# Kernel optimization log

Hardware: AMD Instinct MI355X
Metric: run time of the kernel (lower is better)

The kernel has to match this reference:

```python
import jax, jax.numpy as jnp
import numpy as np

N_NODES = 100000
N_EDGES = 3200000
D_IN = 16
D_OUT = 32


def setup_inputs() -> dict:
    key = jax.random.key(0)
    ks = jax.random.split(key, 8)
    x = jax.random.normal(ks[0], (N_NODES, D_IN), dtype=jnp.float32)
    edge_index = jax.random.randint(ks[1], (2, N_EDGES), 0, N_NODES, dtype=jnp.int64)
    s = 1.0 / np.sqrt(D_IN)
    # mlp1: Linear(16,16) -> ReLU -> Linear(16,16)
    w1 = jax.random.uniform(ks[2], (D_IN, D_IN), jnp.float32, -s, s)
    b1 = jax.random.uniform(ks[3], (D_IN,), jnp.float32, -s, s)
    w2 = jax.random.uniform(ks[4], (D_IN, D_IN), jnp.float32, -s, s)
    b2 = jax.random.uniform(ks[5], (D_IN,), jnp.float32, -s, s)
    # SAGEConv(16,32): lin_l (neighbors, with bias), lin_r (root, no bias)
    wl = jax.random.uniform(ks[6], (D_IN, D_OUT), jnp.float32, -s, s)
    bl = jnp.zeros((D_OUT,), jnp.float32)
    wr = jax.random.uniform(ks[7], (D_IN, D_OUT), jnp.float32, -s, s)
    return {"x": x, "edge_index": edge_index, "w1": w1, "b1": b1,
            "w2": w2, "b2": b2, "wl": wl, "bl": bl, "wr": wr}


def reference(x, edge_index, w1, b1, w2, b2, wl, bl, wr):
    # MLP: Linear -> ReLU -> Linear
    h = jax.nn.relu(x @ w1 + b1) @ w2 + b2  # [N, 16]
    src, dst = edge_index[0], edge_index[1]
    # mean aggregation of neighbor (source) features at destination nodes
    msg = h[src]  # [E, 16]
    summed = jax.ops.segment_sum(msg, dst, num_segments=N_NODES)  # [N, 16]
    cnt = jax.ops.segment_sum(jnp.ones((msg.shape[0],), h.dtype), dst,
                              num_segments=N_NODES)
    mean = summed / jnp.maximum(cnt, 1.0)[:, None]
    # SAGEConv: lin_l(aggr) + lin_r(root)
    out = mean @ wl + bl + h @ wr  # [N, 32]
    return out
```

## Files before the change

### kernel.cpp

```cpp
#include <hip/hip_runtime.h>
#include <hip/hip_bf16.h>

#define D_IN_C 16
#define BUCKET_SHIFT 9
#define BUCKET_NODES 512
#define CAP 18432
#define PT 16
#define PART_CHUNK 4096

__global__ __launch_bounds__(256) void mlp_kernel(
    const float* __restrict__ x,
    const float* __restrict__ w1, const float* __restrict__ b1,
    const float* __restrict__ w2, const float* __restrict__ b2,
    float* __restrict__ h, int* __restrict__ bcur,
    int n_nodes) {
  __shared__ float sw1[256];
  __shared__ float sw2[256];
  __shared__ float sb1[16];
  __shared__ float sb2[16];
  int t = threadIdx.x;
  if (blockIdx.x == 0) bcur[t] = 0;
  sw1[t] = w1[t];
  sw2[t] = w2[t];
  if (t < 16) { sb1[t] = b1[t]; sb2[t] = b2[t]; }
  __syncthreads();

  int n = blockIdx.x * blockDim.x + t;
  if (n >= n_nodes) return;

  float xi[16];
  const float4* xr = (const float4*)(x + (size_t)n * 16);
  float4 v0 = xr[0], v1 = xr[1], v2 = xr[2], v3 = xr[3];
  xi[0]=v0.x; xi[1]=v0.y; xi[2]=v0.z; xi[3]=v0.w;
  xi[4]=v1.x; xi[5]=v1.y; xi[6]=v1.z; xi[7]=v1.w;
  xi[8]=v2.x; xi[9]=v2.y; xi[10]=v2.z; xi[11]=v2.w;
  xi[12]=v3.x; xi[13]=v3.y; xi[14]=v3.z; xi[15]=v3.w;

  float t1[16];
#pragma unroll
  for (int j = 0; j < 16; ++j) {
    float acc = sb1[j];
#pragma unroll
    for (int k = 0; k < 16; ++k) acc += xi[k] * sw1[k * 16 + j];
    t1[j] = fmaxf(acc, 0.0f);
  }
  float hh[16];
#pragma unroll
  for (int j = 0; j < 16; ++j) {
    float acc = sb2[j];
#pragma unroll
    for (int k = 0; k < 16; ++k) acc += t1[k] * sw2[k * 16 + j];
    hh[j] = acc;
  }

  float4* hw = (float4*)(h + (size_t)n * 16);
  hw[0] = make_float4(hh[0], hh[1], hh[2], hh[3]);
  hw[1] = make_float4(hh[4], hh[5], hh[6], hh[7]);
  hw[2] = make_float4(hh[8], hh[9], hh[10], hh[11]);
  hw[3] = make_float4(hh[12], hh[13], hh[14], hh[15]);
}

__global__ __launch_bounds__(256) void part_kernel(
    const int* __restrict__ src, const int* __restrict__ dst,
    int* __restrict__ bcur, int* __restrict__ part,
    int* __restrict__ cnt, int nbuck, int n_edges) {
  __shared__ int lhist[256];
  __shared__ int lofs[256];
  int t = threadIdx.x;
  int base = blockIdx.x * PART_CHUNK;

  int zi = blockIdx.x * 256 + t;
  if (zi < nbuck * BUCKET_NODES) cnt[zi] = 0;

  if (t < nbuck) lhist[t] = 0;
  __syncthreads();

  int d[PT], s[PT];
#pragma unroll
  for (int i = 0; i < PT; ++i) {
    int e = base + i * 256 + t;
    if (e < n_edges) { d[i] = dst[e]; s[i] = src[e]; }
    else d[i] = -1;
  }
#pragma unroll
  for (int i = 0; i < PT; ++i) {
    if (d[i] >= 0) atomicAdd(&lhist[d[i] >> BUCKET_SHIFT], 1);
  }
  __syncthreads();
  if (t < nbuck) {
    int c = lhist[t];
    int r = (c > 0) ? atomicAdd(&bcur[t], c) : 0;
    lofs[t] = t * CAP + r;
  }
  __syncthreads();
#pragma unroll
  for (int i = 0; i < PT; ++i) {
    if (d[i] >= 0) {
      int b = d[i] >> BUCKET_SHIFT;
      int p = atomicAdd(&lofs[b], 1);
      part[p] = ((d[i] & (BUCKET_NODES - 1)) << 17) | s[i];
    }
  }
}

__global__ __launch_bounds__(512, 6) void acc_kernel(
    const float* __restrict__ h, const int* __restrict__ part,
    const int* __restrict__ bcur, int* __restrict__ cnt,
    float* __restrict__ partial,
    int nbuck, int C) {
  __shared__ float acc[BUCKET_NODES * 16];
  __shared__ int dcnt[BUCKET_NODES];
  int t = threadIdx.x;
  int b = blockIdx.x / C;
  int c = blockIdx.x % C;

#pragma unroll
  for (int i = t; i < BUCKET_NODES * 16; i += 512) acc[i] = 0.0f;
  dcnt[t] = 0;
  __syncthreads();

  int count = bcur[b];
  int start = b * CAP + (int)((long long)count * c / C);
  int end   = b * CAP + (int)((long long)count * (c + 1) / C);

  int g = t >> 4;
  int k = t & 15;

  int nfull = (end - start) >> 8;
  int e = start;
  for (int f = 0; f < nfull; ++f, e += 256) {
    int pk[8];
#pragma unroll
    for (int u = 0; u < 8; ++u) pk[u] = part[e + u * 32 + g];
    float v[8];
#pragma unroll
    for (int u = 0; u < 8; ++u)
      v[u] = h[((unsigned)(pk[u] & 0x1FFFF) << 4) | (unsigned)k];
#pragma unroll
    for (int u = 0; u < 8; ++u) {
      unsigned dl = (unsigned)pk[u] >> 17;
      atomicAdd(&acc[(dl << 4) | (unsigned)k], v[u]);
      if (k == 0) atomicAdd(&dcnt[dl], 1);
    }
  }
  for (int ee = e + g; ee < end; ee += 32) {
    int pk = part[ee];
    float v = h[((unsigned)(pk & 0x1FFFF) << 4) | (unsigned)k];
    unsigned dl = (unsigned)pk >> 17;
    atomicAdd(&acc[(dl << 4) | (unsigned)k], v);
    if (k == 0) atomicAdd(&dcnt[dl], 1);
  }
  __syncthreads();

  float* pout = partial + (size_t)c * nbuck * BUCKET_NODES * 16
                        + (size_t)b * BUCKET_NODES * 16;
  float4* pout4 = (float4*)pout;
  const float4* a4 = (const float4*)acc;
#pragma unroll
  for (int i = t; i < BUCKET_NODES * 4; i += 512) pout4[i] = a4[i];
  int dc = dcnt[t];
  if (dc) atomicAdd(&cnt[b * BUCKET_NODES + t], dc);
}

__global__ __launch_bounds__(256) void out_kernel(
    const float* __restrict__ h, const float* __restrict__ partial,
    const int* __restrict__ cnt,
    const float* __restrict__ wl, const float* __restrict__ bl,
    const float* __restrict__ wr, float* __restrict__ out,
    int n_nodes, int nbuck, int C) {
  __shared__ float swl[512];
  __shared__ float swr[512];
  __shared__ float sbl[32];
  int t = threadIdx.x;
  for (int i = t; i < 512; i += 256) { swl[i] = wl[i]; swr[i] = wr[i]; }
  if (t < 32) sbl[t] = bl[t];
  __syncthreads();

  int n = blockIdx.x * 256 + t;
  if (n >= n_nodes) return;

  size_t stride = (size_t)nbuck * BUCKET_NODES * 16;
  float mean[16];
#pragma unroll
  for (int k = 0; k < 16; ++k) mean[k] = 0.0f;
  for (int c = 0; c < C; ++c) {
    const float4* pr = (const float4*)(partial + c * stride + (size_t)n * 16);
    float4 p0 = pr[0], p1 = pr[1], p2 = pr[2], p3 = pr[3];
    mean[0]+=p0.x; mean[1]+=p0.y; mean[2]+=p0.z; mean[3]+=p0.w;
    mean[4]+=p1.x; mean[5]+=p1.y; mean[6]+=p1.z; mean[7]+=p1.w;
    mean[8]+=p2.x; mean[9]+=p2.y; mean[10]+=p2.z; mean[11]+=p2.w;
    mean[12]+=p3.x; mean[13]+=p3.y; mean[14]+=p3.z; mean[15]+=p3.w;
  }
  float inv = 1.0f / fmaxf((float)cnt[n], 1.0f);
#pragma unroll
  for (int k = 0; k < 16; ++k) mean[k] *= inv;

  float hr[16];
  const float4* hp = (const float4*)(h + (size_t)n * 16);
  float4 h0 = hp[0], h1 = hp[1], h2 = hp[2], h3 = hp[3];
  hr[0]=h0.x; hr[1]=h0.y; hr[2]=h0.z; hr[3]=h0.w;
  hr[4]=h1.x; hr[5]=h1.y; hr[6]=h1.z; hr[7]=h1.w;
  hr[8]=h2.x; hr[9]=h2.y; hr[10]=h2.z; hr[11]=h2.w;
  hr[12]=h3.x; hr[13]=h3.y; hr[14]=h3.z; hr[15]=h3.w;

  float o[32];
#pragma unroll
  for (int j = 0; j < 32; ++j) o[j] = sbl[j];
#pragma unroll
  for (int k = 0; k < 16; ++k) {
#pragma unroll
    for (int j = 0; j < 32; ++j) {
      o[j] += mean[k] * swl[k * 32 + j] + hr[k] * swr[k * 32 + j];
    }
  }
  float4* ow = (float4*)(out + (size_t)n * 32);
#pragma unroll
  for (int q = 0; q < 8; ++q)
    ow[q] = make_float4(o[q*4], o[q*4+1], o[q*4+2], o[q*4+3]);
}

extern "C" void kernel_launch(void* const* d_in, const int* in_sizes, int n_in,
                              void* d_out, int out_size, void* d_ws, size_t ws_size,
                              hipStream_t stream) {
  const float* x  = (const float*)d_in[0];
  const int* eidx = (const int*)d_in[1];
  const float* w1 = (const float*)d_in[2];
  const float* b1 = (const float*)d_in[3];
  const float* w2 = (const float*)d_in[4];
  const float* b2 = (const float*)d_in[5];
  const float* wl = (const float*)d_in[6];
  const float* bl = (const float*)d_in[7];
  const float* wr = (const float*)d_in[8];
  float* out = (float*)d_out;

  const int n_nodes = in_sizes[0] / D_IN_C;
  const int n_edges = in_sizes[1] / 2;
  const int* src = eidx;
  const int* dst = eidx + n_edges;

  const int nbuck = (n_nodes + BUCKET_NODES - 1) / BUCKET_NODES;

  float* h     = (float*)d_ws;
  int* part    = (int*)(h + (size_t)n_nodes * 16);
  int* bcur    = part + (size_t)nbuck * CAP;
  int* cnt     = bcur + 256;
  float* partial = (float*)(cnt + (size_t)nbuck * BUCKET_NODES);

  size_t fixed = (size_t)n_nodes * 16 * 4 + (size_t)nbuck * CAP * 4
               + 256 * 4 + (size_t)nbuck * BUCKET_NODES * 4;
  size_t per_copy = (size_t)nbuck * BUCKET_NODES * 16 * 4;
  int C = 2;
  if (ws_size >= fixed + 8 * per_copy) C = 8;
  else if (ws_size >= fixed + 4 * per_copy) C = 4;

  mlp_kernel<<<(n_nodes + 255) / 256, 256, 0, stream>>>(
      x, w1, b1, w2, b2, h, bcur, n_nodes);
  part_kernel<<<(n_edges + PART_CHUNK - 1) / PART_CHUNK, 256, 0, stream>>>(
      src, dst, bcur, part, cnt, nbuck, n_edges);
  acc_kernel<<<nbuck * C, 512, 0, stream>>>(
      h, part, bcur, cnt, partial, nbuck, C);
  out_kernel<<<(n_nodes + 255) / 256, 256, 0, stream>>>(
      h, partial, cnt, wl, bl, wr, out, n_nodes, nbuck, C);
}
```

Measured before the change: 444.2 us.

## Vectorize edge-packet loads with inline asm and shrink accumulate blocks

The accumulation kernel now uses 256-thread blocks, with each 16-lane group reading 8 consecutive packed edges via two dwordx4 loads in inline assembly. It then issues eight batched gathers of h before doing the LDS atomics. Chunk boundaries are aligned to 8 edges, and the split factor C is capped at 4 to reduce partial-sum traffic. The asm waits on vmcnt(0) after each batch, which may serialize latency. Halving threads per block also lowers per-CU occupancy for the same shared-memory footprint.

Result: slower. 482.8 us (+8.7%).

```diff
diff --git a/kernel.cpp b/kernel.cpp
--- a/kernel.cpp
+++ b/kernel.cpp
@@ -7,6 +7,8 @@
 #define CAP 18432
 #define PT 16
 #define PART_CHUNK 4096
+
+typedef int v4i __attribute__((ext_vector_type(4)));
 
 __global__ __launch_bounds__(256) void mlp_kernel(
     const float* __restrict__ x,
@@ -103,7 +105,7 @@
   }
 }
 
-__global__ __launch_bounds__(512, 6) void acc_kernel(
+__global__ __launch_bounds__(256, 4) void acc_kernel(
     const float* __restrict__ h, const int* __restrict__ part,
     const int* __restrict__ bcur, int* __restrict__ cnt,
     float* __restrict__ partial,
@@ -114,38 +116,84 @@
   int b = blockIdx.x / C;
   int c = blockIdx.x % C;
 
-#pragma unroll
-  for (int i = t; i < BUCKET_NODES * 16; i += 512) acc[i] = 0.0f;
+  float4* accz = (float4*)acc;
+#pragma unroll
+  for (int i = t; i < BUCKET_NODES * 4; i += 256)
+    accz[i] = make_float4(0.f, 0.f, 0.f, 0.f);
   dcnt[t] = 0;
+  dcnt[t + 256] = 0;
   __syncthreads();
 
   int count = bcur[b];
-  int start = b * CAP + (int)((long long)count * c / C);
-  int end   = b * CAP + (int)((long long)count * (c + 1) / C);
+  int s0 = (int)((long long)count * c / C) & ~7;
+  int s1 = (c + 1 == C) ? count : ((int)((long long)count * (c + 1) / C) & ~7);
+  int start = b * CAP + s0;
+  int end   = b * CAP + s1;
 
   int g = t >> 4;
   int k = t & 15;
 
-  int nfull = (end - start) >> 8;
+  int nfull = (end - start) >> 7;
   int e = start;
-  for (int f = 0; f < nfull; ++f, e += 256) {
-    int pk[8];
-#pragma unroll
-    for (int u = 0; u < 8; ++u) pk[u] = part[e + u * 32 + g];
-    float v[8];
-#pragma unroll
-    for (int u = 0; u < 8; ++u)
-      v[u] = h[((unsigned)(pk[u] & 0x1FFFF) << 4) | (unsigned)k];
-#pragma unroll
-    for (int u = 0; u < 8; ++u) {
-      unsigned dl = (unsigned)pk[u] >> 17;
-      atomicAdd(&acc[(dl << 4) | (unsigned)k], v[u]);
-      if (k == 0) atomicAdd(&dcnt[dl], 1);
+  for (int f = 0; f < nfull; ++f, e += 128) {
+    const int* pp = part + e + g * 8;
+    v4i pa, pb;
+    asm volatile(
+        "global_load_dwordx4 %0, %[q0], off\n\t"
+        "global_load_dwordx4 %1, %[q1], off\n\t"
+        "s_waitcnt vmcnt(0)"
+        : "=&v"(pa), "=&v"(pb)
+        : [q0] "v"(pp), [q1] "v"(pp + 4)
+        : "memory");
+
+    const float* p0 = h + ((((unsigned)pa.x & 0x1FFFFu) << 4) | (unsigned)k);
+    const float* p1 = h + ((((unsigned)pa.y & 0x1FFFFu) << 4) | (unsigned)k);
+    const float* p2 = h + ((((unsigned)pa.z & 0x1FFFFu) << 4) | (unsigned)k);
+    const float* p3 = h + ((((unsigned)pa.w & 0x1FFFFu) << 4) | (unsigned)k);
+    const float* p4 = h + ((((unsigned)pb.x & 0x1FFFFu) << 4) | (unsigned)k);
+    const float* p5 = h + ((((unsigned)pb.y & 0x1FFFFu) << 4) | (unsigned)k);
+    const float* p6 = h + ((((unsigned)pb.z & 0x1FFFFu) << 4) | (unsigned)k);
+    const float* p7 = h + ((((unsigned)pb.w & 0x1FFFFu) << 4) | (unsigned)k);
+
+    float v0, v1, v2, v3, v4, v5, v6, v7;
+    asm volatile(
+        "global_load_dword %0, %[a0], off\n\t"
+        "global_load_dword %1, %[a1], off\n\t"
+        "global_load_dword %2, %[a2], off\n\t"
+        "global_load_dword %3, %[a3], off\n\t"
+        "global_load_dword %4, %[a4], off\n\t"
+        "global_load_dword %5, %[a5], off\n\t"
+        "global_load_dword %6, %[a6], off\n\t"
+        "global_load_dword %7, %[a7], off\n\t"
+        "s_waitcnt vmcnt(0)"
+        : "=&v"(v0), "=&v"(v1), "=&v"(v2), "=&v"(v3),
+          "=&v"(v4), "=&v"(v5), "=&v"(v6), "=&v"(v7)
+        : [a0] "v"(p0), [a1] "v"(p1), [a2] "v"(p2), [a3] "v"(p3),
+          [a4] "v"(p4), [a5] "v"(p5), [a6] "v"(p6), [a7] "v"(p7)
+        : "memory");
+
+    atomicAdd(&acc[((((unsigned)pa.x) >> 17) << 4) | (unsigned)k], v0);
+    atomicAdd(&acc[((((unsigned)pa.y) >> 17) << 4) | (unsigned)k], v1);
+    atomicAdd(&acc[((((unsigned)pa.z) >> 17) << 4) | (unsigned)k], v2);
+    atomicAdd(&acc[((((unsigned)pa.w) >> 17) << 4) | (unsigned)k], v3);
+    atomicAdd(&acc[((((unsigned)pb.x) >> 17) << 4) | (unsigned)k], v4);
+    atomicAdd(&acc[((((unsigned)pb.y) >> 17) << 4) | (unsigned)k], v5);
+    atomicAdd(&acc[((((unsigned)pb.z) >> 17) << 4) | (unsigned)k], v6);
+    atomicAdd(&acc[((((unsigned)pb.w) >> 17) << 4) | (unsigned)k], v7);
+    if (k == 0) {
+      atomicAdd(&dcnt[(unsigned)pa.x >> 17], 1);
+      atomicAdd(&dcnt[(unsigned)pa.y >> 17], 1);
+      atomicAdd(&dcnt[(unsigned)pa.z >> 17], 1);
+      atomicAdd(&dcnt[(unsigned)pa.w >> 17], 1);
+      atomicAdd(&dcnt[(unsigned)pb.x >> 17], 1);
+      atomicAdd(&dcnt[(unsigned)pb.y >> 17], 1);
+      atomicAdd(&dcnt[(unsigned)pb.z >> 17], 1);
+      atomicAdd(&dcnt[(unsigned)pb.w >> 17], 1);
     }
   }
-  for (int ee = e + g; ee < end; ee += 32) {
+  for (int ee = e + g; ee < end; ee += 16) {
     int pk = part[ee];
-    float v = h[((unsigned)(pk & 0x1FFFF) << 4) | (unsigned)k];
+    float v = h[(((unsigned)pk & 0x1FFFFu) << 4) | (unsigned)k];
     unsigned dl = (unsigned)pk >> 17;
     atomicAdd(&acc[(dl << 4) | (unsigned)k], v);
     if (k == 0) atomicAdd(&dcnt[dl], 1);
@@ -157,9 +205,10 @@
   float4* pout4 = (float4*)pout;
   const float4* a4 = (const float4*)acc;
 #pragma unroll
-  for (int i = t; i < BUCKET_NODES * 4; i += 512) pout4[i] = a4[i];
-  int dc = dcnt[t];
-  if (dc) atomicAdd(&cnt[b * BUCKET_NODES + t], dc);
+  for (int i = t; i < BUCKET_NODES * 4; i += 256) pout4[i] = a4[i];
+  int n0 = b * BUCKET_NODES + t;
+  if (dcnt[t]) atomicAdd(&cnt[n0], dcnt[t]);
+  if (dcnt[t + 256]) atomicAdd(&cnt[n0 + 256], dcnt[t + 256]);
 }
 
 __global__ __launch_bounds__(256) void out_kernel(
@@ -249,15 +298,13 @@
   size_t fixed = (size_t)n_nodes * 16 * 4 + (size_t)nbuck * CAP * 4
                + 256 * 4 + (size_t)nbuck * BUCKET_NODES * 4;
   size_t per_copy = (size_t)nbuck * BUCKET_NODES * 16 * 4;
-  int C = 2;
-  if (ws_size >= fixed + 8 * per_copy) C = 8;
-  else if (ws_size >= fixed + 4 * per_copy) C = 4;
+  int C = (ws_size >= fixed + 4 * per_copy) ? 4 : 2;
 
   mlp_kernel<<<(n_nodes + 255) / 256, 256, 0, stream>>>(
       x, w1, b1, w2, b2, h, bcur, n_nodes);
   part_kernel<<<(n_edges + PART_CHUNK - 1) / PART_CHUNK, 256, 0, stream>>>(
       src, dst, bcur, part, cnt, nbuck, n_edges);
-  acc_kernel<<<nbuck * C, 512, 0, stream>>>(
+  acc_kernel<<<nbuck * C, 256, 0, stream>>>(
       h, part, bcur, cnt, partial, nbuck, C);
   out_kernel<<<(n_nodes + 255) / 256, 256, 0, stream>>>(
       h, partial, cnt, wl, bl, wr, out, n_nodes, nbuck, C);
```

## Partition edges by source range within destination buckets for gather locality

Applied to the files above, without the earlier changes.

Edges are binned into sub-buckets keyed by destination bucket and one of four source-node ranges. Each accumulation block processes one sub-bucket, so its gathers of h touch only a quarter of the node table. Blocks are ordered so that those running together share a source range, which should improve cache hit rates. In exchange, the partition histogram is larger, there are more global offset atomics, and the split factor is fixed at four instead of adapting to workspace size.

New measurement: 488.2 us. 9.9% more time.

```diff
diff --git a/kernel.cpp b/kernel.cpp
--- a/kernel.cpp
+++ b/kernel.cpp
@@ -4,9 +4,12 @@
 #define D_IN_C 16
 #define BUCKET_SHIFT 9
 #define BUCKET_NODES 512
-#define CAP 18432
+#define SRC_SHIFT 15
+#define NSRC 4
+#define SUBCAP 6144
 #define PT 16
 #define PART_CHUNK 4096
+#define MAXSUB 1024
 
 __global__ __launch_bounds__(256) void mlp_kernel(
     const float* __restrict__ x,
@@ -19,7 +22,7 @@
   __shared__ float sb1[16];
   __shared__ float sb2[16];
   int t = threadIdx.x;
-  if (blockIdx.x == 0) bcur[t] = 0;
+  if (blockIdx.x < MAXSUB / 256) bcur[blockIdx.x * 256 + t] = 0;
   sw1[t] = w1[t];
   sw2[t] = w2[t];
   if (t < 16) { sb1[t] = b1[t]; sb2[t] = b2[t]; }
@@ -63,16 +66,16 @@
 __global__ __launch_bounds__(256) void part_kernel(
     const int* __restrict__ src, const int* __restrict__ dst,
     int* __restrict__ bcur, int* __restrict__ part,
-    int* __restrict__ cnt, int nbuck, int n_edges) {
-  __shared__ int lhist[256];
-  __shared__ int lofs[256];
+    int* __restrict__ cnt, int nsub, int nbuck, int n_edges) {
+  __shared__ int lhist[MAXSUB];
+  __shared__ int lofs[MAXSUB];
   int t = threadIdx.x;
   int base = blockIdx.x * PART_CHUNK;
 
   int zi = blockIdx.x * 256 + t;
   if (zi < nbuck * BUCKET_NODES) cnt[zi] = 0;
 
-  if (t < nbuck) lhist[t] = 0;
+  for (int i = t; i < nsub; i += 256) lhist[i] = 0;
   __syncthreads();
 
   int d[PT], s[PT];
@@ -84,20 +87,23 @@
   }
 #pragma unroll
   for (int i = 0; i < PT; ++i) {
-    if (d[i] >= 0) atomicAdd(&lhist[d[i] >> BUCKET_SHIFT], 1);
-  }
-  __syncthreads();
-  if (t < nbuck) {
-    int c = lhist[t];
-    int r = (c > 0) ? atomicAdd(&bcur[t], c) : 0;
-    lofs[t] = t * CAP + r;
+    if (d[i] >= 0) {
+      int sb = ((d[i] >> BUCKET_SHIFT) << 2) | (s[i] >> SRC_SHIFT);
+      atomicAdd(&lhist[sb], 1);
+    }
+  }
+  __syncthreads();
+  for (int i = t; i < nsub; i += 256) {
+    int c = lhist[i];
+    int r = (c > 0) ? atomicAdd(&bcur[i], c) : 0;
+    lofs[i] = i * SUBCAP + r;
   }
   __syncthreads();
 #pragma unroll
   for (int i = 0; i < PT; ++i) {
     if (d[i] >= 0) {
-      int b = d[i] >> BUCKET_SHIFT;
-      int p = atomicAdd(&lofs[b], 1);
+      int sb = ((d[i] >> BUCKET_SHIFT) << 2) | (s[i] >> SRC_SHIFT);
+      int p = atomicAdd(&lofs[sb], 1);
       part[p] = ((d[i] & (BUCKET_NODES - 1)) << 17) | s[i];
     }
   }
@@ -107,26 +113,29 @@
     const float* __restrict__ h, const int* __restrict__ part,
     const int* __restrict__ bcur, int* __restrict__ cnt,
     float* __restrict__ partial,
-    int nbuck, int C) {
+    int nbuck) {
   __shared__ float acc[BUCKET_NODES * 16];
   __shared__ int dcnt[BUCKET_NODES];
   int t = threadIdx.x;
-  int b = blockIdx.x / C;
-  int c = blockIdx.x % C;
-
-#pragma unroll
-  for (int i = t; i < BUCKET_NODES * 16; i += 512) acc[i] = 0.0f;
+  int c = blockIdx.x / nbuck;
+  int b = blockIdx.x % nbuck;
+
+  float4* accz = (float4*)acc;
+#pragma unroll
+  for (int i = t; i < BUCKET_NODES * 4; i += 512)
+    accz[i] = make_float4(0.f, 0.f, 0.f, 0.f);
   dcnt[t] = 0;
   __syncthreads();
 
-  int count = bcur[b];
-  int start = b * CAP + (int)((long long)count * c / C);
-  int end   = b * CAP + (int)((long long)count * (c + 1) / C);
+  int sub = b * NSRC + c;
+  int count = bcur[sub];
+  int start = sub * SUBCAP;
+  int end = start + count;
 
   int g = t >> 4;
   int k = t & 15;
 
-  int nfull = (end - start) >> 8;
+  int nfull = count >> 8;
   int e = start;
   for (int f = 0; f < nfull; ++f, e += 256) {
     int pk[8];
@@ -167,7 +176,7 @@
     const int* __restrict__ cnt,
     const float* __restrict__ wl, const float* __restrict__ bl,
     const float* __restrict__ wr, float* __restrict__ out,
-    int n_nodes, int nbuck, int C) {
+    int n_nodes, int nbuck) {
   __shared__ float swl[512];
   __shared__ float swr[512];
   __shared__ float sbl[32];
@@ -183,7 +192,7 @@
   float mean[16];
 #pragma unroll
   for (int k = 0; k < 16; ++k) mean[k] = 0.0f;
-  for (int c = 0; c < C; ++c) {
+  for (int c = 0; c < NSRC; ++c) {
     const float4* pr = (const float4*)(partial + c * stride + (size_t)n * 16);
     float4 p0 = pr[0], p1 = pr[1], p2 = pr[2], p3 = pr[3];
     mean[0]+=p0.x; mean[1]+=p0.y; mean[2]+=p0.z; mean[3]+=p0.w;
@@ -239,26 +248,20 @@
   const int* dst = eidx + n_edges;
 
   const int nbuck = (n_nodes + BUCKET_NODES - 1) / BUCKET_NODES;
+  const int nsub = nbuck * NSRC;
 
   float* h     = (float*)d_ws;
   int* part    = (int*)(h + (size_t)n_nodes * 16);
-  int* bcur    = part + (size_t)nbuck * CAP;
-  int* cnt     = bcur + 256;
+  int* bcur    = part + (size_t)nsub * SUBCAP;
+  int* cnt     = bcur + MAXSUB;
   float* partial = (float*)(cnt + (size_t)nbuck * BUCKET_NODES);
-
-  size_t fixed = (size_t)n_nodes * 16 * 4 + (size_t)nbuck * CAP * 4
-               + 256 * 4 + (size_t)nbuck * BUCKET_NODES * 4;
-  size_t per_copy = (size_t)nbuck * BUCKET_NODES * 16 * 4;
-  int C = 2;
-  if (ws_size >= fixed + 8 * per_copy) C = 8;
-  else if (ws_size >= fixed + 4 * per_copy) C = 4;
 
   mlp_kernel<<<(n_nodes + 255) / 256, 256, 0, stream>>>(
       x, w1, b1, w2, b2, h, bcur, n_nodes);
   part_kernel<<<(n_edges + PART_CHUNK - 1) / PART_CHUNK, 256, 0, stream>>>(
-      src, dst, bcur, part, cnt, nbuck, n_edges);
-  acc_kernel<<<nbuck * C, 512, 0, stream>>>(
-      h, part, bcur, cnt, partial, nbuck, C);
+      src, dst, bcur, part, cnt, nsub, nbuck, n_edges);
+  acc_kernel<<<NSRC * nbuck, 512, 0, stream>>>(
+      h, part, bcur, cnt, partial, nbuck);
   out_kernel<<<(n_nodes + 255) / 256, 256, 0, stream>>>(
-      h, partial, cnt, wl, bl, wr, out, n_nodes, nbuck, C);
-}
+      h, partial, cnt, wl, bl, wr, out, n_nodes, nbuck);
+}
```
